# Kernel optimization log

Measured on AMD Instinct MI355X. Metric: run time of the kernel, lower is better.

Reference implementation:

```python
import jax, jax.numpy as jnp
import numpy as np

N_NODES = 100000
N_EDGES = 1600000
NODE_DIM = 32
MSG_DIM = 32
COORD_DIM = 3
FF_HALF = 4  # FourierLayer(1, 8) -> coeff [1, 4]


def silu(x):
    return x * jax.nn.sigmoid(x)


def setup_inputs() -> dict:
    key = jax.random.key(0)
    ks = jax.random.split(key, 16)
    s = lambda fan_in: 1.0 / np.sqrt(fan_in)
    edge_in = 2 * NODE_DIM + 2 * FF_HALF  # 72
    node_in = MSG_DIM + NODE_DIM          # 64
    return {
        "coord": jax.random.normal(ks[0], (N_NODES, COORD_DIM), jnp.float32),
        "node_feat": jax.random.normal(ks[1], (N_NODES, NODE_DIM), jnp.float32),
        "edge_index": jax.random.randint(ks[2], (2, N_EDGES), 0, N_NODES, jnp.int64 if jax.config.jax_enable_x64 else jnp.int32),
        "ff_coeff": jax.random.normal(ks[3], (1, FF_HALF), jnp.float32),  # sigma=1.0
        "ew1": jax.random.uniform(ks[4], (edge_in, MSG_DIM), jnp.float32, -s(edge_in), s(edge_in)),
        "eb1": jax.random.uniform(ks[5], (MSG_DIM,), jnp.float32, -s(edge_in), s(edge_in)),
        "ew2": jax.random.uniform(ks[6], (MSG_DIM, MSG_DIM), jnp.float32, -s(MSG_DIM), s(MSG_DIM)),
        "eb2": jax.random.uniform(ks[7], (MSG_DIM,), jnp.float32, -s(MSG_DIM), s(MSG_DIM)),
        "cw1": jax.random.uniform(ks[8], (MSG_DIM, MSG_DIM), jnp.float32, -s(MSG_DIM), s(MSG_DIM)),
        "cb1": jax.random.uniform(ks[9], (MSG_DIM,), jnp.float32, -s(MSG_DIM), s(MSG_DIM)),
        "cw2": jax.random.uniform(ks[10], (MSG_DIM, 1), jnp.float32, -s(MSG_DIM), s(MSG_DIM)),  # bias-free last coord layer
        "nw1": jax.random.uniform(ks[11], (node_in, MSG_DIM), jnp.float32, -s(node_in), s(node_in)),
        "nb1": jax.random.uniform(ks[12], (MSG_DIM,), jnp.float32, -s(node_in), s(node_in)),
        "nw2": jax.random.uniform(ks[13], (MSG_DIM, NODE_DIM), jnp.float32, -s(MSG_DIM), s(MSG_DIM)),
        "nb2": jax.random.uniform(ks[14], (NODE_DIM,), jnp.float32, -s(MSG_DIM), s(MSG_DIM)),
    }


def reference(coord, node_feat, edge_index, ff_coeff, ew1, eb1, ew2, eb2,
              cw1, cb1, cw2, nw1, nb1, nw2, nb2):
    n = coord.shape[0]
    idx_i, idx_j = edge_index[0], edge_index[1]
    # coord2radial (sparse, normalize=False)
    coord_diff = coord[idx_i] - coord[idx_j]                 # [E, 3]
    radial = jnp.sum(coord_diff * coord_diff, axis=1, keepdims=True)  # [E, 1]
    # Fourier radial features (ffr=True): ff1(radial) -> [E, 8]
    x_proj = (2.0 * jnp.pi) * (radial @ ff_coeff)            # [E, 4]
    ff = jnp.concatenate([jnp.cos(x_proj), jnp.sin(x_proj)], axis=-1)  # [E, 8]
    # edge MLP
    edge_in = jnp.concatenate([node_feat[idx_i], node_feat[idx_j], ff], axis=1)  # [E, 72]
    m = silu(edge_in @ ew1 + eb1)
    m = silu(m @ ew2 + eb2)                                  # [E, M]
    # coord model: per-edge scalar weight on coord_diff, mean-aggregated to nodes
    w = silu(m @ cw1 + cb1) @ cw2                            # [E, 1]
    trans = coord_diff * w                                   # [E, 3]
    agg_c = jax.ops.segment_sum(trans, idx_i, num_segments=n)
    counts = jax.ops.segment_sum(jnp.ones((trans.shape[0],), trans.dtype), idx_i, num_segments=n)
    coord_out = coord + agg_c / jnp.clip(counts, 1.0)[:, None]
    # node model: sum-aggregated messages, residual
    agg_h = jax.ops.segment_sum(m, idx_i, num_segments=n)    # [N, M]
    h = silu(jnp.concatenate([node_feat, agg_h], axis=1) @ nw1 + nb1)
    h = h @ nw2 + nb2
    node_out = node_feat + h                                 # is_residual=True
    return node_out, coord_out
```

## Files before the change

### kernel.cpp

```cpp
#include <hip/hip_runtime.h>
#include <math.h>

__device__ __forceinline__ float silu_f(float x) {
    return x / (1.0f + __expf(-x));
}

__device__ __forceinline__ void sincos_2pi_rev(float rev, float& s, float& c) {
#if __has_builtin(__builtin_amdgcn_sinf) && __has_builtin(__builtin_amdgcn_cosf)
    const float fr = rev - floorf(rev);
    s = __builtin_amdgcn_sinf(fr);
    c = __builtin_amdgcn_cosf(fr);
#else
    const float xp = 6.2831853071795864769f * rev;
    s = sinf(xp); c = cosf(xp);
#endif
}

__device__ __forceinline__ void edge_core(
    const float* __restrict__ coord,
    const float* __restrict__ node_feat,
    const float* __restrict__ ff_coeff,
    const float* __restrict__ ew1, const float* __restrict__ eb1,
    const float* __restrict__ ew2, const float* __restrict__ eb2,
    const float* __restrict__ cw1, const float* __restrict__ cb1,
    const float* __restrict__ cw2,
    int i, int j,
    float* __restrict__ m,
    float& cdx, float& cdy, float& cdz, float& w)
{
    const float cix = coord[3*(size_t)i+0], ciy = coord[3*(size_t)i+1], ciz = coord[3*(size_t)i+2];
    const float cjx = coord[3*(size_t)j+0], cjy = coord[3*(size_t)j+1], cjz = coord[3*(size_t)j+2];
    cdx = cix - cjx; cdy = ciy - cjy; cdz = ciz - cjz;
    const float radial = cdx*cdx + cdy*cdy + cdz*cdz;

    float ff[8];
    #pragma unroll
    for (int k = 0; k < 4; ++k) {
        float s, c;
        sincos_2pi_rev(radial * ff_coeff[k], s, c);
        ff[k]     = c;
        ff[4 + k] = s;
    }

    float acc[32];
    #pragma unroll
    for (int o = 0; o < 32; ++o) acc[o] = eb1[o];

    {
        const float4* nfi4 = reinterpret_cast<const float4*>(node_feat + (size_t)i * 32);
        for (int q = 0; q < 8; ++q) {
            float4 v = nfi4[q];
            float xs[4] = {v.x, v.y, v.z, v.w};
            const float* wr = ew1 + q * 4 * 32;
            #pragma unroll
            for (int kk = 0; kk < 4; ++kk) {
                #pragma unroll
                for (int o = 0; o < 32; ++o)
                    acc[o] = fmaf(xs[kk], wr[kk*32 + o], acc[o]);
            }
        }
        const float4* nfj4 = reinterpret_cast<const float4*>(node_feat + (size_t)j * 32);
        for (int q = 0; q < 8; ++q) {
            float4 v = nfj4[q];
            float xs[4] = {v.x, v.y, v.z, v.w};
            const float* wr = ew1 + (32 + q * 4) * 32;
            #pragma unroll
            for (int kk = 0; kk < 4; ++kk) {
                #pragma unroll
                for (int o = 0; o < 32; ++o)
                    acc[o] = fmaf(xs[kk], wr[kk*32 + o], acc[o]);
            }
        }
        #pragma unroll
        for (int k = 0; k < 8; ++k) {
            const float* wr = ew1 + (64 + k) * 32;
            #pragma unroll
            for (int o = 0; o < 32; ++o)
                acc[o] = fmaf(ff[k], wr[o], acc[o]);
        }
    }

    float m1[32];
    #pragma unroll
    for (int o = 0; o < 32; ++o) m1[o] = silu_f(acc[o]);

    #pragma unroll
    for (int o = 0; o < 32; ++o) m[o] = eb2[o];
    #pragma unroll
    for (int h = 0; h < 32; ++h) {
        #pragma unroll
        for (int o = 0; o < 32; ++o)
            m[o] = fmaf(m1[h], ew2[h*32 + o], m[o]);
    }
    #pragma unroll
    for (int o = 0; o < 32; ++o) m[o] = silu_f(m[o]);

    float c1[32];
    #pragma unroll
    for (int o = 0; o < 32; ++o) c1[o] = cb1[o];
    #pragma unroll
    for (int h = 0; h < 32; ++h) {
        #pragma unroll
        for (int o = 0; o < 32; ++o)
            c1[o] = fmaf(m[h], cw1[h*32 + o], c1[o]);
    }
    w = 0.0f;
    #pragma unroll
    for (int o = 0; o < 32; ++o) w += silu_f(c1[o]) * cw2[o];
}


__global__ __launch_bounds__(256) void egc_hist(
    const int* __restrict__ idx_i, int* __restrict__ counts, int E)
{
    const int e = blockIdx.x * 256 + threadIdx.x;
    if (e < E) atomicAdd(&counts[idx_i[e]], 1);
}

__global__ __launch_bounds__(1024) void egc_scan(
    const int* __restrict__ counts, int* __restrict__ row_start,
    int* __restrict__ cursor, int N)
{
    __shared__ int wsum[16];
    __shared__ int carry_s;
    const int tid = threadIdx.x;
    const int lane = tid & 63, wid = tid >> 6;
    if (tid == 0) carry_s = 0;
    __syncthreads();
    for (int base = 0; base < N; base += 1024) {
        const int idx = base + tid;
        const int x = (idx < N) ? counts[idx] : 0;
        int incl = x;
        #pragma unroll
        for (int off = 1; off < 64; off <<= 1) {
            int v = __shfl_up(incl, off, 64);
            if (lane >= off) incl += v;
        }
        if (lane == 63) wsum[wid] = incl;
        __syncthreads();
        if (wid == 0) {
            int v = (lane < 16) ? wsum[lane] : 0;
            int s = v;
            #pragma unroll
            for (int off = 1; off < 16; off <<= 1) {
                int t = __shfl_up(s, off, 64);
                if (lane >= off) s += t;
            }
            if (lane < 16) wsum[lane] = s - v;
        }
        __syncthreads();
        const int carry = carry_s;
        if (idx < N) {
            const int v = carry + wsum[wid] + incl - x;
            row_start[idx] = v;
            cursor[idx]    = v;
        }
        __syncthreads();
        if (tid == 1023) carry_s = carry + wsum[15] + incl;
        __syncthreads();
    }
    if (tid == 0) row_start[N] = carry_s;
}

__global__ __launch_bounds__(256) void egc_edge_direct(
    const float* __restrict__ coord,
    const float* __restrict__ node_feat,
    const int*   __restrict__ edge_index,
    const float* __restrict__ ff_coeff,
    const float* __restrict__ ew1, const float* __restrict__ eb1,
    const float* __restrict__ ew2, const float* __restrict__ eb2,
    const float* __restrict__ cw1, const float* __restrict__ cb1,
    const float* __restrict__ cw2,
    int*   __restrict__ cursor,
    float* __restrict__ m_buf,
    float* __restrict__ trans4,
    int*   __restrict__ eord,
    int E)
{
    const int e = blockIdx.x * 256 + threadIdx.x;
    if (e >= E) return;

    const int i = edge_index[e];
    const int j = edge_index[E + e];
    const int slot = atomicAdd(&cursor[i], 1);

    float m[32], cdx, cdy, cdz, w;
    edge_core(coord, node_feat, ff_coeff, ew1, eb1, ew2, eb2, cw1, cb1, cw2,
              i, j, m, cdx, cdy, cdz, w);

    float4* mb = reinterpret_cast<float4*>(m_buf + (size_t)slot * 32);
    #pragma unroll
    for (int q = 0; q < 8; ++q) {
        float4 v;
        v.x = m[4*q+0]; v.y = m[4*q+1]; v.z = m[4*q+2]; v.w = m[4*q+3];
        mb[q] = v;
    }
    float4 t; t.x = cdx * w; t.y = cdy * w; t.z = cdz * w; t.w = 0.0f;
    *reinterpret_cast<float4*>(trans4 + (size_t)e * 4) = t;
    eord[slot] = e;
}

__global__ __launch_bounds__(256) void egc_node_wave(
    const float* __restrict__ coord,
    const float* __restrict__ node_feat,
    const float* __restrict__ m_buf,
    const float* __restrict__ trans4,
    const int*   __restrict__ eord,
    const int*   __restrict__ row_start,
    const float* __restrict__ nw1, const float* __restrict__ nb1,
    const float* __restrict__ nw2, const float* __restrict__ nb2,
    float* __restrict__ out_node,
    float* __restrict__ out_coord,
    int N)
{
    const int tid = threadIdx.x;
    const int l32 = tid & 31;
    const int n = blockIdx.x * 8 + (tid >> 5);
    if (n >= N) return;

    const int rs = row_start[n];
    const int re = row_start[n + 1];

    float agg = 0.0f;
    float tr  = 0.0f;
    for (int k = rs; k < re; ++k) {
        agg += m_buf[(size_t)k * 32 + l32];
        if (l32 < 3) {
            const int e = eord[k];
            tr += trans4[(size_t)e * 4 + l32];
        }
    }

    const float nf = node_feat[(size_t)n * 32 + l32];

    float acc = nb1[l32];
    #pragma unroll
    for (int k = 0; k < 32; ++k)
        acc = fmaf(__shfl(nf, k, 32), nw1[k*32 + l32], acc);
    #pragma unroll
    for (int k = 0; k < 32; ++k)
        acc = fmaf(__shfl(agg, k, 32), nw1[(32+k)*32 + l32], acc);
    const float h1 = silu_f(acc);

    float h2 = nb2[l32];
    #pragma unroll
    for (int k = 0; k < 32; ++k)
        h2 = fmaf(__shfl(h1, k, 32), nw2[k*32 + l32], h2);

    out_node[(size_t)n * 32 + l32] = nf + h2;

    if (l32 < 3) {
        const float deg = (float)(re - rs);
        out_coord[(size_t)n * 3 + l32] =
            coord[(size_t)n * 3 + l32] + tr / fmaxf(deg, 1.0f);
    }
}


__global__ __launch_bounds__(256) void egc_edge_fb(
    const float* __restrict__ coord,
    const float* __restrict__ node_feat,
    const int*   __restrict__ edge_index,
    const float* __restrict__ ff_coeff,
    const float* __restrict__ ew1, const float* __restrict__ eb1,
    const float* __restrict__ ew2, const float* __restrict__ eb2,
    const float* __restrict__ cw1, const float* __restrict__ cb1,
    const float* __restrict__ cw2,
    float* __restrict__ agg_h, float* __restrict__ agg_c, float* __restrict__ counts,
    int E)
{
    const int e = blockIdx.x * 256 + threadIdx.x;
    if (e >= E) return;
    const int i = edge_index[e];
    const int j = edge_index[E + e];

    float m[32], cdx, cdy, cdz, w;
    edge_core(coord, node_feat, ff_coeff, ew1, eb1, ew2, eb2, cw1, cb1, cw2,
              i, j, m, cdx, cdy, cdz, w);

    float* dst = agg_h + (size_t)i * 32;
    #pragma unroll
    for (int o = 0; o < 32; ++o) atomicAdd(&dst[o], m[o]);
    atomicAdd(&agg_c[(size_t)i*3 + 0], cdx * w);
    atomicAdd(&agg_c[(size_t)i*3 + 1], cdy * w);
    atomicAdd(&agg_c[(size_t)i*3 + 2], cdz * w);
    atomicAdd(&counts[i], 1.0f);
}

__global__ __launch_bounds__(256) void egc_node_fb(
    const float* __restrict__ coord,
    const float* __restrict__ node_feat,
    const float* __restrict__ agg_h,
    const float* __restrict__ agg_c,
    const float* __restrict__ counts,
    const float* __restrict__ nw1, const float* __restrict__ nb1,
    const float* __restrict__ nw2, const float* __restrict__ nb2,
    float* __restrict__ out_node, float* __restrict__ out_coord, int N)
{
    const int n = blockIdx.x * 256 + threadIdx.x;
    if (n >= N) return;

    float nf[32];
    {
        const float4* nf4 = reinterpret_cast<const float4*>(node_feat + (size_t)n * 32);
        #pragma unroll
        for (int q = 0; q < 8; ++q) {
            float4 v = nf4[q];
            nf[4*q+0] = v.x; nf[4*q+1] = v.y; nf[4*q+2] = v.z; nf[4*q+3] = v.w;
        }
    }
    float acc[32];
    #pragma unroll
    for (int o = 0; o < 32; ++o) acc[o] = nb1[o];
    #pragma unroll
    for (int k = 0; k < 32; ++k) {
        #pragma unroll
        for (int o = 0; o < 32; ++o)
            acc[o] = fmaf(nf[k], nw1[k*32 + o], acc[o]);
    }
    {
        const float4* ah4 = reinterpret_cast<const float4*>(agg_h + (size_t)n * 32);
        #pragma unroll
        for (int q = 0; q < 8; ++q) {
            float4 v = ah4[q];
            float xs[4] = {v.x, v.y, v.z, v.w};
            const float* wr = nw1 + (32 + q * 4) * 32;
            #pragma unroll
            for (int kk = 0; kk < 4; ++kk) {
                #pragma unroll
                for (int o = 0; o < 32; ++o)
                    acc[o] = fmaf(xs[kk], wr[kk*32 + o], acc[o]);
            }
        }
    }
    float h1[32];
    #pragma unroll
    for (int o = 0; o < 32; ++o) h1[o] = silu_f(acc[o]);
    float h2[32];
    #pragma unroll
    for (int o = 0; o < 32; ++o) h2[o] = nb2[o];
    #pragma unroll
    for (int k = 0; k < 32; ++k) {
        #pragma unroll
        for (int o = 0; o < 32; ++o)
            h2[o] = fmaf(h1[k], nw2[k*32 + o], h2[o]);
    }
    {
        float4* on4 = reinterpret_cast<float4*>(out_node + (size_t)n * 32);
        #pragma unroll
        for (int q = 0; q < 8; ++q) {
            float4 v;
            v.x = nf[4*q+0] + h2[4*q+0];
            v.y = nf[4*q+1] + h2[4*q+1];
            v.z = nf[4*q+2] + h2[4*q+2];
            v.w = nf[4*q+3] + h2[4*q+3];
            on4[q] = v;
        }
    }
    const float cnt = fmaxf(counts[n], 1.0f);
    const float inv = 1.0f / cnt;
    out_coord[(size_t)n*3 + 0] = coord[(size_t)n*3 + 0] + agg_c[(size_t)n*3 + 0] * inv;
    out_coord[(size_t)n*3 + 1] = coord[(size_t)n*3 + 1] + agg_c[(size_t)n*3 + 1] * inv;
    out_coord[(size_t)n*3 + 2] = coord[(size_t)n*3 + 2] + agg_c[(size_t)n*3 + 2] * inv;
}


extern "C" void kernel_launch(void* const* d_in, const int* in_sizes, int n_in,
                              void* d_out, int out_size, void* d_ws, size_t ws_size,
                              hipStream_t stream) {
    const float* coord     = (const float*)d_in[0];
    const float* node_feat = (const float*)d_in[1];
    const int*   edge_index= (const int*)  d_in[2];
    const float* ff_coeff  = (const float*)d_in[3];
    const float* ew1 = (const float*)d_in[4];
    const float* eb1 = (const float*)d_in[5];
    const float* ew2 = (const float*)d_in[6];
    const float* eb2 = (const float*)d_in[7];
    const float* cw1 = (const float*)d_in[8];
    const float* cb1 = (const float*)d_in[9];
    const float* cw2 = (const float*)d_in[10];
    const float* nw1 = (const float*)d_in[11];
    const float* nb1 = (const float*)d_in[12];
    const float* nw2 = (const float*)d_in[13];
    const float* nb2 = (const float*)d_in[14];

    const int N = in_sizes[0] / 3;
    const int E = in_sizes[2] / 2;

    float* out_node  = (float*)d_out;
    float* out_coord = out_node + (size_t)N * 32;

    const size_t m_off   = 0;
    const size_t t_off   = m_off + (size_t)E * 32;
    const size_t eo_off  = t_off + (size_t)E * 4;
    const size_t cnt_off = eo_off + (size_t)E;
    const size_t cur_off = cnt_off + (size_t)N;
    const size_t rs_off  = cur_off + (size_t)N;
    const size_t need_bytes = (rs_off + (size_t)N + 1) * 4 + 256;

    if (ws_size >= need_bytes) {
        float* m_buf     = (float*)d_ws + m_off;
        float* trans4    = (float*)d_ws + t_off;
        int*   eord      = (int*)d_ws + eo_off;
        int*   counts    = (int*)d_ws + cnt_off;
        int*   cursor    = (int*)d_ws + cur_off;
        int*   row_start = (int*)d_ws + rs_off;

        hipMemsetAsync(counts, 0, (size_t)N * sizeof(int), stream);

        egc_hist<<<(E + 255) / 256, 256, 0, stream>>>(edge_index, counts, E);

        egc_scan<<<1, 1024, 0, stream>>>(counts, row_start, cursor, N);

        egc_edge_direct<<<(E + 255) / 256, 256, 0, stream>>>(
            coord, node_feat, edge_index, ff_coeff,
            ew1, eb1, ew2, eb2, cw1, cb1, cw2,
            cursor, m_buf, trans4, eord, E);

        egc_node_wave<<<(N + 7) / 8, 256, 0, stream>>>(
            coord, node_feat, m_buf, trans4, eord, row_start,
            nw1, nb1, nw2, nb2, out_node, out_coord, N);
    } else {
        float* agg_h  = (float*)d_ws;
        float* agg_c  = agg_h + (size_t)N * 32;
        float* counts = agg_c + (size_t)N * 3;
        hipMemsetAsync(d_ws, 0, (size_t)N * 36 * sizeof(float), stream);

        egc_edge_fb<<<(E + 255) / 256, 256, 0, stream>>>(
            coord, node_feat, edge_index, ff_coeff,
            ew1, eb1, ew2, eb2, cw1, cb1, cw2,
            agg_h, agg_c, counts, E);

        egc_node_fb<<<(N + 255) / 256, 256, 0, stream>>>(
            coord, node_feat, agg_h, agg_c, counts,
            nw1, nb1, nw2, nb2, out_node, out_coord, N);
    }
}
```

Before: 861.3 us.

## Precompute per-node first-layer projections and decouple CSR scatter from edge MLP

The first edge-MLP layer is split algebraically: each node's contributions from node_feat through ew1 (the i-part with bias and the j-part) are computed once per node into Pi/Pj. The edge kernel then gathers and adds two 32-float vectors instead of doing 64x32 FMAs per edge. CSR slot assignment moves to a separate scatter kernel, so m_buf is written in edge order and the node kernel reads it indirectly through eord. The scan also processes four counts per thread, and the fallback node kernel becomes wave-per-node. This costs extra node-sized buffers, another launch, and uncoalesced gathers of m_buf in the node kernel.

```diff
diff --git a/kernel.cpp b/kernel.cpp
--- a/kernel.cpp
+++ b/kernel.cpp
@@ -16,99 +16,28 @@
 #endif
 }
 
-__device__ __forceinline__ void edge_core(
-    const float* __restrict__ coord,
+__global__ __launch_bounds__(256) void egc_proj(
     const float* __restrict__ node_feat,
-    const float* __restrict__ ff_coeff,
     const float* __restrict__ ew1, const float* __restrict__ eb1,
-    const float* __restrict__ ew2, const float* __restrict__ eb2,
-    const float* __restrict__ cw1, const float* __restrict__ cb1,
-    const float* __restrict__ cw2,
-    int i, int j,
-    float* __restrict__ m,
-    float& cdx, float& cdy, float& cdz, float& w)
-{
-    const float cix = coord[3*(size_t)i+0], ciy = coord[3*(size_t)i+1], ciz = coord[3*(size_t)i+2];
-    const float cjx = coord[3*(size_t)j+0], cjy = coord[3*(size_t)j+1], cjz = coord[3*(size_t)j+2];
-    cdx = cix - cjx; cdy = ciy - cjy; cdz = ciz - cjz;
-    const float radial = cdx*cdx + cdy*cdy + cdz*cdz;
-
-    float ff[8];
-    #pragma unroll
-    for (int k = 0; k < 4; ++k) {
-        float s, c;
-        sincos_2pi_rev(radial * ff_coeff[k], s, c);
-        ff[k]     = c;
-        ff[4 + k] = s;
-    }
-
-    float acc[32];
-    #pragma unroll
-    for (int o = 0; o < 32; ++o) acc[o] = eb1[o];
-
-    {
-        const float4* nfi4 = reinterpret_cast<const float4*>(node_feat + (size_t)i * 32);
-        for (int q = 0; q < 8; ++q) {
-            float4 v = nfi4[q];
-            float xs[4] = {v.x, v.y, v.z, v.w};
-            const float* wr = ew1 + q * 4 * 32;
-            #pragma unroll
-            for (int kk = 0; kk < 4; ++kk) {
-                #pragma unroll
-                for (int o = 0; o < 32; ++o)
-                    acc[o] = fmaf(xs[kk], wr[kk*32 + o], acc[o]);
-            }
-        }
-        const float4* nfj4 = reinterpret_cast<const float4*>(node_feat + (size_t)j * 32);
-        for (int q = 0; q < 8; ++q) {
-            float4 v = nfj4[q];
-            float xs[4] = {v.x, v.y, v.z, v.w};
-            const float* wr = ew1 + (32 + q * 4) * 32;
-            #pragma unroll
-            for (int kk = 0; kk < 4; ++kk) {
-                #pragma unroll
-                for (int o = 0; o < 32; ++o)
-                    acc[o] = fmaf(xs[kk], wr[kk*32 + o], acc[o]);
-            }
-        }
-        #pragma unroll
-        for (int k = 0; k < 8; ++k) {
-            const float* wr = ew1 + (64 + k) * 32;
-            #pragma unroll
-            for (int o = 0; o < 32; ++o)
-                acc[o] = fmaf(ff[k], wr[o], acc[o]);
-        }
-    }
-
-    float m1[32];
-    #pragma unroll
-    for (int o = 0; o < 32; ++o) m1[o] = silu_f(acc[o]);
-
-    #pragma unroll
-    for (int o = 0; o < 32; ++o) m[o] = eb2[o];
-    #pragma unroll
-    for (int h = 0; h < 32; ++h) {
-        #pragma unroll
-        for (int o = 0; o < 32; ++o)
-            m[o] = fmaf(m1[h], ew2[h*32 + o], m[o]);
-    }
-    #pragma unroll
-    for (int o = 0; o < 32; ++o) m[o] = silu_f(m[o]);
-
-    float c1[32];
-    #pragma unroll
-    for (int o = 0; o < 32; ++o) c1[o] = cb1[o];
-    #pragma unroll
-    for (int h = 0; h < 32; ++h) {
-        #pragma unroll
-        for (int o = 0; o < 32; ++o)
-            c1[o] = fmaf(m[h], cw1[h*32 + o], c1[o]);
-    }
-    w = 0.0f;
-    #pragma unroll
-    for (int o = 0; o < 32; ++o) w += silu_f(c1[o]) * cw2[o];
-}
-
+    float* __restrict__ Pi, float* __restrict__ Pj, int N)
+{
+    const int tid = threadIdx.x;
+    const int l32 = tid & 31;
+    const int n = blockIdx.x * 8 + (tid >> 5);
+    if (n >= N) return;
+
+    const float nf = node_feat[(size_t)n * 32 + l32];
+    float pi = eb1[l32];
+    float pj = 0.0f;
+    #pragma unroll
+    for (int k = 0; k < 32; ++k) {
+        const float b = __shfl(nf, k, 32);
+        pi = fmaf(b, ew1[k * 32 + l32], pi);
+        pj = fmaf(b, ew1[(32 + k) * 32 + l32], pj);
+    }
+    Pi[(size_t)n * 32 + l32] = pi;
+    Pj[(size_t)n * 32 + l32] = pj;
+}
 
 __global__ __launch_bounds__(256) void egc_hist(
     const int* __restrict__ idx_i, int* __restrict__ counts, int E)
@@ -127,10 +56,19 @@
     const int lane = tid & 63, wid = tid >> 6;
     if (tid == 0) carry_s = 0;
     __syncthreads();
-    for (int base = 0; base < N; base += 1024) {
-        const int idx = base + tid;
-        const int x = (idx < N) ? counts[idx] : 0;
-        int incl = x;
+    for (int base = 0; base < N; base += 4096) {
+        const int i0 = base + tid * 4;
+        int v0 = 0, v1 = 0, v2 = 0, v3 = 0;
+        if (i0 + 3 < N) {
+            const int4 q = *reinterpret_cast<const int4*>(counts + i0);
+            v0 = q.x; v1 = q.y; v2 = q.z; v3 = q.w;
+        } else {
+            if (i0 + 0 < N) v0 = counts[i0 + 0];
+            if (i0 + 1 < N) v1 = counts[i0 + 1];
+            if (i0 + 2 < N) v2 = counts[i0 + 2];
+        }
+        const int p1 = v0, p2 = v0 + v1, p3 = v0 + v1 + v2, tot = p3 + v3;
+        int incl = tot;
         #pragma unroll
         for (int off = 1; off < 64; off <<= 1) {
             int v = __shfl_up(incl, off, 64);
@@ -150,11 +88,11 @@
         }
         __syncthreads();
         const int carry = carry_s;
-        if (idx < N) {
-            const int v = carry + wsum[wid] + incl - x;
-            row_start[idx] = v;
-            cursor[idx]    = v;
-        }
+        const int tb = carry + wsum[wid] + incl - tot;
+        if (i0 + 0 < N) { row_start[i0 + 0] = tb;      cursor[i0 + 0] = tb; }
+        if (i0 + 1 < N) { row_start[i0 + 1] = tb + p1; cursor[i0 + 1] = tb + p1; }
+        if (i0 + 2 < N) { row_start[i0 + 2] = tb + p2; cursor[i0 + 2] = tb + p2; }
+        if (i0 + 3 < N) { row_start[i0 + 3] = tb + p3; cursor[i0 + 3] = tb + p3; }
         __syncthreads();
         if (tid == 1023) carry_s = carry + wsum[15] + incl;
         __syncthreads();
@@ -162,7 +100,112 @@
     if (tid == 0) row_start[N] = carry_s;
 }
 
-__global__ __launch_bounds__(256) void egc_edge_direct(
+__global__ __launch_bounds__(256) void egc_scatter(
+    const int* __restrict__ idx_i, int* __restrict__ cursor,
+    int* __restrict__ eord, int E)
+{
+    const int e = blockIdx.x * 256 + threadIdx.x;
+    if (e >= E) return;
+    const int slot = atomicAdd(&cursor[idx_i[e]], 1);
+    eord[slot] = e;
+}
+
+__global__ __launch_bounds__(256) void egc_edge_proj(
+    const float* __restrict__ coord,
+    const int*   __restrict__ edge_index,
+    const float* __restrict__ ff_coeff,
+    const float* __restrict__ Pi, const float* __restrict__ Pj,
+    const float* __restrict__ ew1,
+    const float* __restrict__ ew2, const float* __restrict__ eb2,
+    const float* __restrict__ cw1, const float* __restrict__ cb1,
+    const float* __restrict__ cw2,
+    float* __restrict__ m_buf,
+    float* __restrict__ trans4,
+    int E)
+{
+    const int e = blockIdx.x * 256 + threadIdx.x;
+    if (e >= E) return;
+
+    const int i = edge_index[e];
+    const int j = edge_index[E + e];
+
+    const float cix = coord[3*(size_t)i+0], ciy = coord[3*(size_t)i+1], ciz = coord[3*(size_t)i+2];
+    const float cjx = coord[3*(size_t)j+0], cjy = coord[3*(size_t)j+1], cjz = coord[3*(size_t)j+2];
+    const float cdx = cix - cjx, cdy = ciy - cjy, cdz = ciz - cjz;
+    const float radial = cdx*cdx + cdy*cdy + cdz*cdz;
+
+    float ff[8];
+    #pragma unroll
+    for (int k = 0; k < 4; ++k) {
+        float s, c;
+        sincos_2pi_rev(radial * ff_coeff[k], s, c);
+        ff[k]     = c;
+        ff[4 + k] = s;
+    }
+
+    float acc[32];
+    {
+        const float4* a4 = reinterpret_cast<const float4*>(Pi + (size_t)i * 32);
+        const float4* b4 = reinterpret_cast<const float4*>(Pj + (size_t)j * 32);
+        #pragma unroll
+        for (int q = 0; q < 8; ++q) {
+            const float4 x = a4[q], y = b4[q];
+            acc[4*q+0] = x.x + y.x;
+            acc[4*q+1] = x.y + y.y;
+            acc[4*q+2] = x.z + y.z;
+            acc[4*q+3] = x.w + y.w;
+        }
+    }
+    #pragma unroll
+    for (int k = 0; k < 8; ++k) {
+        const float* wr = ew1 + (64 + k) * 32;
+        #pragma unroll
+        for (int o = 0; o < 32; ++o)
+            acc[o] = fmaf(ff[k], wr[o], acc[o]);
+    }
+
+    float m1[32];
+    #pragma unroll
+    for (int o = 0; o < 32; ++o) m1[o] = silu_f(acc[o]);
+
+    float m[32];
+    #pragma unroll
+    for (int o = 0; o < 32; ++o) m[o] = eb2[o];
+    #pragma unroll
+    for (int h = 0; h < 32; ++h) {
+        #pragma unroll
+        for (int o = 0; o < 32; ++o)
+            m[o] = fmaf(m1[h], ew2[h*32 + o], m[o]);
+    }
+    #pragma unroll
+    for (int o = 0; o < 32; ++o) m[o] = silu_f(m[o]);
+
+    float4* mb = reinterpret_cast<float4*>(m_buf + (size_t)e * 32);
+    #pragma unroll
+    for (int q = 0; q < 8; ++q) {
+        float4 v;
+        v.x = m[4*q+0]; v.y = m[4*q+1]; v.z = m[4*q+2]; v.w = m[4*q+3];
+        mb[q] = v;
+    }
+
+    float c1[32];
+    #pragma unroll
+    for (int o = 0; o < 32; ++o) c1[o] = cb1[o];
+    #pragma unroll
+    for (int h = 0; h < 32; ++h) {
+        #pragma unroll
+        for (int o = 0; o < 32; ++o)
+            c1[o] = fmaf(m[h], cw1[h*32 + o], c1[o]);
+    }
+    float w = 0.0f;
+    #pragma unroll
+    for (int o = 0; o < 32; ++o) w += silu_f(c1[o]) * cw2[o];
+
+    float4 t; t.x = cdx * w; t.y = cdy * w; t.z = cdz * w; t.w = 0.0f;
+    *reinterpret_cast<float4*>(trans4 + (size_t)e * 4) = t;
+}
+
+__global__ __launch_bounds__(256) void egc_edge_full(
     const float* __restrict__ coord,
     const float* __restrict__ node_feat,
     const int*   __restrict__ edge_index,
@@ -171,33 +214,97 @@
     const float* __restrict__ ew2, const float* __restrict__ eb2,
     const float* __restrict__ cw1, const float* __restrict__ cb1,
     const float* __restrict__ cw2,
-    int*   __restrict__ cursor,
-    float* __restrict__ m_buf,
-    float* __restrict__ trans4,
-    int*   __restrict__ eord,
-    int E)
+    float* __restrict__ m_buf, float* __restrict__ trans4, int E)
 {
     const int e = blockIdx.x * 256 + threadIdx.x;
     if (e >= E) return;
 
     const int i = edge_index[e];
     const int j = edge_index[E + e];
-    const int slot = atomicAdd(&cursor[i], 1);
-
-    float m[32], cdx, cdy, cdz, w;
-    edge_core(coord, node_feat, ff_coeff, ew1, eb1, ew2, eb2, cw1, cb1, cw2,
-              i, j, m, cdx, cdy, cdz, w);
-
-    float4* mb = reinterpret_cast<float4*>(m_buf + (size_t)slot * 32);
+
+    const float cix = coord[3*(size_t)i+0], ciy = coord[3*(size_t)i+1], ciz = coord[3*(size_t)i+2];
+    const float cjx = coord[3*(size_t)j+0], cjy = coord[3*(size_t)j+1], cjz = coord[3*(size_t)j+2];
+    const float cdx = cix - cjx, cdy = ciy - cjy, cdz = ciz - cjz;
+    const float radial = cdx*cdx + cdy*cdy + cdz*cdz;
+
+    float ff[8];
+    #pragma unroll
+    for (int k = 0; k < 4; ++k) {
+        float s, c;
+        sincos_2pi_rev(radial * ff_coeff[k], s, c);
+        ff[k] = c; ff[4+k] = s;
+    }
+
+    float acc[32];
+    #pragma unroll
+    for (int o = 0; o < 32; ++o) acc[o] = eb1[o];
+    {
+        const float4* nfi4 = reinterpret_cast<const float4*>(node_feat + (size_t)i * 32);
+        for (int q = 0; q < 8; ++q) {
+            float4 v = nfi4[q];
+            float xs[4] = {v.x, v.y, v.z, v.w};
+            const float* wr = ew1 + q * 4 * 32;
+            #pragma unroll
+            for (int kk = 0; kk < 4; ++kk)
+                #pragma unroll
+                for (int o = 0; o < 32; ++o)
+                    acc[o] = fmaf(xs[kk], wr[kk*32 + o], acc[o]);
+        }
+        const float4* nfj4 = reinterpret_cast<const float4*>(node_feat + (size_t)j * 32);
+        for (int q = 0; q < 8; ++q) {
+            float4 v = nfj4[q];
+            float xs[4] = {v.x, v.y, v.z, v.w};
+            const float* wr = ew1 + (32 + q * 4) * 32;
+            #pragma unroll
+            for (int kk = 0; kk < 4; ++kk)
+                #pragma unroll
+                for (int o = 0; o < 32; ++o)
+                    acc[o] = fmaf(xs[kk], wr[kk*32 + o], acc[o]);
+        }
+        #pragma unroll
+        for (int k = 0; k < 8; ++k) {
+            const float* wr = ew1 + (64 + k) * 32;
+            #pragma unroll
+            for (int o = 0; o < 32; ++o)
+                acc[o] = fmaf(ff[k], wr[o], acc[o]);
+        }
+    }
+    float m1[32];
+    #pragma unroll
+    for (int o = 0; o < 32; ++o) m1[o] = silu_f(acc[o]);
+    float m[32];
+    #pragma unroll
+    for (int o = 0; o < 32; ++o) m[o] = eb2[o];
+    #pragma unroll
+    for (int h = 0; h < 32; ++h)
+        #pragma unroll
+        for (int o = 0; o < 32; ++o)
+            m[o] = fmaf(m1[h], ew2[h*32 + o], m[o]);
+    #pragma unroll
+    for (int o = 0; o < 32; ++o) m[o] = silu_f(m[o]);
+
+    float4* mb = reinterpret_cast<float4*>(m_buf + (size_t)e * 32);
     #pragma unroll
     for (int q = 0; q < 8; ++q) {
         float4 v;
         v.x = m[4*q+0]; v.y = m[4*q+1]; v.z = m[4*q+2]; v.w = m[4*q+3];
         mb[q] = v;
     }
+
+    float c1[32];
+    #pragma unroll
+    for (int o = 0; o < 32; ++o) c1[o] = cb1[o];
+    #pragma unroll
+    for (int h = 0; h < 32; ++h)
+        #pragma unroll
+        for (int o = 0; o < 32; ++o)
+            c1[o] = fmaf(m[h], cw1[h*32 + o], c1[o]);
+    float w = 0.0f;
+    #pragma unroll
+    for (int o = 0; o < 32; ++o) w += silu_f(c1[o]) * cw2[o];
+
     float4 t; t.x = cdx * w; t.y = cdy * w; t.z = cdz * w; t.w = 0.0f;
     *reinterpret_cast<float4*>(trans4 + (size_t)e * 4) = t;
-    eord[slot] = e;
 }
 
 __global__ __launch_bounds__(256) void egc_node_wave(
@@ -209,9 +316,7 @@
     const int*   __restrict__ row_start,
     const float* __restrict__ nw1, const float* __restrict__ nb1,
     const float* __restrict__ nw2, const float* __restrict__ nb2,
-    float* __restrict__ out_node,
-    float* __restrict__ out_coord,
-    int N)
+    float* __restrict__ out_node, float* __restrict__ out_coord, int N)
 {
     const int tid = threadIdx.x;
     const int l32 = tid & 31;
@@ -224,11 +329,9 @@
     float agg = 0.0f;
     float tr  = 0.0f;
     for (int k = rs; k < re; ++k) {
-        agg += m_buf[(size_t)k * 32 + l32];
-        if (l32 < 3) {
-            const int e = eord[k];
-            tr += trans4[(size_t)e * 4 + l32];
-        }
+        const int e = eord[k];
+        agg += m_buf[(size_t)e * 32 + l32];
+        if (l32 < 3) tr += trans4[(size_t)e * 4 + l32];
     }
 
     const float nf = node_feat[(size_t)n * 32 + l32];
@@ -255,7 +358,6 @@
             coord[(size_t)n * 3 + l32] + tr / fmaxf(deg, 1.0f);
     }
 }
-
 
 __global__ __launch_bounds__(256) void egc_edge_fb(
     const float* __restrict__ coord,
@@ -274,13 +376,82 @@
     const int i = edge_index[e];
     const int j = edge_index[E + e];
 
-    float m[32], cdx, cdy, cdz, w;
-    edge_core(coord, node_feat, ff_coeff, ew1, eb1, ew2, eb2, cw1, cb1, cw2,
-              i, j, m, cdx, cdy, cdz, w);
+    const float cix = coord[3*(size_t)i+0], ciy = coord[3*(size_t)i+1], ciz = coord[3*(size_t)i+2];
+    const float cjx = coord[3*(size_t)j+0], cjy = coord[3*(size_t)j+1], cjz = coord[3*(size_t)j+2];
+    const float cdx = cix - cjx, cdy = ciy - cjy, cdz = ciz - cjz;
+    const float radial = cdx*cdx + cdy*cdy + cdz*cdz;
+
+    float ff[8];
+    #pragma unroll
+    for (int k = 0; k < 4; ++k) {
+        float s, c;
+        sincos_2pi_rev(radial * ff_coeff[k], s, c);
+        ff[k] = c; ff[4+k] = s;
+    }
+    float acc[32];
+    #pragma unroll
+    for (int o = 0; o < 32; ++o) acc[o] = eb1[o];
+    {
+        const float4* nfi4 = reinterpret_cast<const float4*>(node_feat + (size_t)i * 32);
+        for (int q = 0; q < 8; ++q) {
+            float4 v = nfi4[q];
+            float xs[4] = {v.x, v.y, v.z, v.w};
+            const float* wr = ew1 + q * 4 * 32;
+            #pragma unroll
+            for (int kk = 0; kk < 4; ++kk)
+                #pragma unroll
+                for (int o = 0; o < 32; ++o)
+                    acc[o] = fmaf(xs[kk], wr[kk*32 + o], acc[o]);
+        }
+        const float4* nfj4 = reinterpret_cast<const float4*>(node_feat + (size_t)j * 32);
+        for (int q = 0; q < 8; ++q) {
+            float4 v = nfj4[q];
+            float xs[4] = {v.x, v.y, v.z, v.w};
+            const float* wr = ew1 + (32 + q * 4) * 32;
+            #pragma unroll
+            for (int kk = 0; kk < 4; ++kk)
+                #pragma unroll
+                for (int o = 0; o < 32; ++o)
+                    acc[o] = fmaf(xs[kk], wr[kk*32 + o], acc[o]);
+        }
+        #pragma unroll
+        for (int k = 0; k < 8; ++k) {
+            const float* wr = ew1 + (64 + k) * 32;
+            #pragma unroll
+            for (int o = 0; o < 32; ++o)
+                acc[o] = fmaf(ff[k], wr[o], acc[o]);
+        }
+    }
+    float m1[32];
+    #pragma unroll
+    for (int o = 0; o < 32; ++o) m1[o] = silu_f(acc[o]);
+    float m[32];
+    #pragma unroll
+    for (int o = 0; o < 32; ++o) m[o] = eb2[o];
+    #pragma unroll
+    for (int h = 0; h < 32; ++h)
+        #pragma unroll
+        for (int o = 0; o < 32; ++o)
+            m[o] = fmaf(m1[h], ew2[h*32 + o], m[o]);
+    #pragma unroll
+    for (int o = 0; o < 32; ++o) m[o] = silu_f(m[o]);
 
     float* dst = agg_h + (size_t)i * 32;
     #pragma unroll
     for (int o = 0; o < 32; ++o) atomicAdd(&dst[o], m[o]);
+
+    float c1[32];
+    #pragma unroll
+    for (int o = 0; o < 32; ++o) c1[o] = cb1[o];
+    #pragma unroll
+    for (int h = 0; h < 32; ++h)
+        #pragma unroll
+        for (int o = 0; o < 32; ++o)
+            c1[o] = fmaf(m[h], cw1[h*32 + o], c1[o]);
+    float w = 0.0f;
+    #pragma unroll
+    for (int o = 0; o < 32; ++o) w += silu_f(c1[o]) * cw2[o];
+
     atomicAdd(&agg_c[(size_t)i*3 + 0], cdx * w);
     atomicAdd(&agg_c[(size_t)i*3 + 1], cdy * w);
     atomicAdd(&agg_c[(size_t)i*3 + 2], cdz * w);
@@ -297,71 +468,35 @@
     const float* __restrict__ nw2, const float* __restrict__ nb2,
     float* __restrict__ out_node, float* __restrict__ out_coord, int N)
 {
-    const int n = blockIdx.x * 256 + threadIdx.x;
+    const int tid = threadIdx.x;
+    const int l32 = tid & 31;
+    const int n = blockIdx.x * 8 + (tid >> 5);
     if (n >= N) return;
 
-    float nf[32];
-    {
-        const float4* nf4 = reinterpret_cast<const float4*>(node_feat + (size_t)n * 32);
-        #pragma unroll
-        for (int q = 0; q < 8; ++q) {
-            float4 v = nf4[q];
-            nf[4*q+0] = v.x; nf[4*q+1] = v.y; nf[4*q+2] = v.z; nf[4*q+3] = v.w;
-        }
-    }
-    float acc[32];
-    #pragma unroll
-    for (int o = 0; o < 32; ++o) acc[o] = nb1[o];
-    #pragma unroll
-    for (int k = 0; k < 32; ++k) {
-        #pragma unroll
-        for (int o = 0; o < 32; ++o)
-            acc[o] = fmaf(nf[k], nw1[k*32 + o], acc[o]);
-    }
-    {
-        const float4* ah4 = reinterpret_cast<const float4*>(agg_h + (size_t)n * 32);
-        #pragma unroll
-        for (int q = 0; q < 8; ++q) {
-            float4 v = ah4[q];
-            float xs[4] = {v.x, v.y, v.z, v.w};
-            const float* wr = nw1 + (32 + q * 4) * 32;
-            #pragma unroll
-            for (int kk = 0; kk < 4; ++kk) {
-                #pragma unroll
-                for (int o = 0; o < 32; ++o)
-                    acc[o] = fmaf(xs[kk], wr[kk*32 + o], acc[o]);
-            }
-        }
-    }
-    float h1[32];
-    #pragma unroll
-    for (int o = 0; o < 32; ++o) h1[o] = silu_f(acc[o]);
-    float h2[32];
-    #pragma unroll
-    for (int o = 0; o < 32; ++o) h2[o] = nb2[o];
-    #pragma unroll
-    for (int k = 0; k < 32; ++k) {
-        #pragma unroll
-        for (int o = 0; o < 32; ++o)
-            h2[o] = fmaf(h1[k], nw2[k*32 + o], h2[o]);
-    }
-    {
-        float4* on4 = reinterpret_cast<float4*>(out_node + (size_t)n * 32);
-        #pragma unroll
-        for (int q = 0; q < 8; ++q) {
-            float4 v;
-            v.x = nf[4*q+0] + h2[4*q+0];
-            v.y = nf[4*q+1] + h2[4*q+1];
-            v.z = nf[4*q+2] + h2[4*q+2];
-            v.w = nf[4*q+3] + h2[4*q+3];
-            on4[q] = v;
-        }
-    }
-    const float cnt = fmaxf(counts[n], 1.0f);
-    const float inv = 1.0f / cnt;
-    out_coord[(size_t)n*3 + 0] = coord[(size_t)n*3 + 0] + agg_c[(size_t)n*3 + 0] * inv;
-    out_coord[(size_t)n*3 + 1] = coord[(size_t)n*3 + 1] + agg_c[(size_t)n*3 + 1] * inv;
-    out_coord[(size_t)n*3 + 2] = coord[(size_t)n*3 + 2] + agg_c[(size_t)n*3 + 2] * inv;
+    const float nf  = node_feat[(size_t)n * 32 + l32];
+    const float agg = agg_h[(size_t)n * 32 + l32];
+
+    float acc = nb1[l32];
+    #pragma unroll
+    for (int k = 0; k < 32; ++k)
+        acc = fmaf(__shfl(nf, k, 32), nw1[k*32 + l32], acc);
+    #pragma unroll
+    for (int k = 0; k < 32; ++k)
+        acc = fmaf(__shfl(agg, k, 32), nw1[(32+k)*32 + l32], acc);
+    const float h1 = silu_f(acc);
+
+    float h2 = nb2[l32];
+    #pragma unroll
+    for (int k = 0; k < 32; ++k)
+        h2 = fmaf(__shfl(h1, k, 32), nw2[k*32 + l32], h2);
+
+    out_node[(size_t)n * 32 + l32] = nf + h2;
+
+    if (l32 < 3) {
+        const float cnt = fmaxf(counts[n], 1.0f);
+        out_coord[(size_t)n * 3 + l32] =
+            coord[(size_t)n * 3 + l32] + agg_c[(size_t)n * 3 + l32] / cnt;
+    }
 }
 
 
@@ -396,9 +531,12 @@
     const size_t cnt_off = eo_off + (size_t)E;
     const size_t cur_off = cnt_off + (size_t)N;
     const size_t rs_off  = cur_off + (size_t)N;
-    const size_t need_bytes = (rs_off + (size_t)N + 1) * 4 + 256;
-
-    if (ws_size >= need_bytes) {
+    const size_t pi_off  = (rs_off + (size_t)N + 1 + 3) & ~(size_t)3;
+    const size_t pj_off  = pi_off + (size_t)N * 32;
+    const size_t need_A  = (pj_off + (size_t)N * 32) * 4 + 256;
+    const size_t need_B  = (rs_off + (size_t)N + 1) * 4 + 256;
+
+    if (ws_size >= need_B) {
         float* m_buf     = (float*)d_ws + m_off;
         float* trans4    = (float*)d_ws + t_off;
         int*   eord      = (int*)d_ws + eo_off;
@@ -409,13 +547,21 @@
         hipMemsetAsync(counts, 0, (size_t)N * sizeof(int), stream);
 
         egc_hist<<<(E + 255) / 256, 256, 0, stream>>>(edge_index, counts, E);
-
         egc_scan<<<1, 1024, 0, stream>>>(counts, row_start, cursor, N);
-
-        egc_edge_direct<<<(E + 255) / 256, 256, 0, stream>>>(
-            coord, node_feat, edge_index, ff_coeff,
-            ew1, eb1, ew2, eb2, cw1, cb1, cw2,
-            cursor, m_buf, trans4, eord, E);
+        egc_scatter<<<(E + 255) / 256, 256, 0, stream>>>(edge_index, cursor, eord, E);
+
+        if (ws_size >= need_A) {
+            float* Pi = (float*)d_ws + pi_off;
+            float* Pj = (float*)d_ws + pj_off;
+            egc_proj<<<(N + 7) / 8, 256, 0, stream>>>(node_feat, ew1, eb1, Pi, Pj, N);
+            egc_edge_proj<<<(E + 255) / 256, 256, 0, stream>>>(
+                coord, edge_index, ff_coeff, Pi, Pj,
+                ew1, ew2, eb2, cw1, cb1, cw2, m_buf, trans4, E);
+        } else {
+            egc_edge_full<<<(E + 255) / 256, 256, 0, stream>>>(
+                coord, node_feat, edge_index, ff_coeff,
+                ew1, eb1, ew2, eb2, cw1, cb1, cw2, m_buf, trans4, E);
+        }
 
         egc_node_wave<<<(N + 7) / 8, 256, 0, stream>>>(
             coord, node_feat, m_buf, trans4, eord, row_start,
@@ -431,7 +577,7 @@
             ew1, eb1, ew2, eb2, cw1, cb1, cw2,
             agg_h, agg_c, counts, E);
 
-        egc_node_fb<<<(N + 255) / 256, 256, 0, stream>>>(
+        egc_node_fb<<<(N + 7) / 8, 256, 0, stream>>>(
             coord, node_feat, agg_h, agg_c, counts,
             nw1, nb1, nw2, nb2, out_node, out_coord, N);
     }
```

Measured after the change: 742.4 us. 13.8% less time.
